# Optimization experiments

Measured on AMD Instinct MI355X. Metric: run time of the kernel, lower is better.

## Reference

```python
import jax, jax.numpy as jnp
import numpy as np

D = 1024
K_LOW1 = D // 4  # first low-precision segment of the contraction dim
K_LOW2 = D // 4  # last low-precision segment


def mix_precision_matmul(x, w):
    """x: [B,N,d], w: [d,3d]. Contraction dim d is split into
    low1 | high | low2 column bands; low bands run in fp16, high in fp32.
    Partial products are summed to give the full matmul result."""
    d = x.shape[-1]
    w1 = w[:K_LOW1]
    wh = w[K_LOW1:d - K_LOW2]
    w2 = w[d - K_LOW2:]
    y1 = jnp.matmul(x[..., :K_LOW1].astype(jnp.float16), w1.astype(jnp.float16)).astype(jnp.float32)
    yh = jnp.matmul(x[..., K_LOW1:d - K_LOW2], wh)
    y2 = jnp.matmul(x[..., d - K_LOW2:].astype(jnp.float16), w2.astype(jnp.float16)).astype(jnp.float32)
    return y1 + yh + y2


def setup_inputs() -> dict:
    key = jax.random.key(0)
    k1, k2, k3, k4 = jax.random.split(key, 4)
    B, N, d = 8, 2048, D
    x = jax.random.normal(k1, (B, N, d), dtype=jnp.float32)
    weight_qkv = jax.random.normal(k2, (d, 3 * d), dtype=jnp.float32) * (d ** -0.5)
    out_w = jax.random.normal(k3, (d, d), dtype=jnp.float32) * (d ** -0.5)
    out_b = jax.random.normal(k4, (d,), dtype=jnp.float32) * 0.01
    return {"x": x, "weight_qkv": weight_qkv, "out_w": out_w, "out_b": out_b}


def reference(x, weight_qkv, out_w, out_b):
    d = x.shape[-1]
    qkv = mix_precision_matmul(x, weight_qkv)  # [B, N, 3d]
    q, k, v = jnp.split(qkv, 3, axis=-1)
    q = q / jnp.sqrt(jnp.asarray(d, dtype=q.dtype))
    qk = jnp.einsum('bqd,bkd->bqk', q, k)      # [B, N, N]
    s = jax.nn.softmax(qk, axis=-1)
    y = jnp.einsum('bqk,bkd->bqd', s, v)       # [B, N, d]
    return jnp.matmul(y, out_w.T) + out_b
```

## Files before the change

kernel.cpp:

```cpp
#include <hip/hip_runtime.h>

typedef unsigned int u32;
typedef __attribute__((ext_vector_type(8))) _Float16 half8;
typedef __attribute__((ext_vector_type(4))) _Float16 half4;
typedef __attribute__((ext_vector_type(4))) float floatx4;

#define DEVI __device__ __forceinline__

DEVI void gload_lds16(const _Float16* g, _Float16* l) {
    __builtin_amdgcn_global_load_lds(
        (const __attribute__((address_space(1))) void*)g,
        (__attribute__((address_space(3))) void*)l, 16, 0, 0);
}

DEVI void stage128(const _Float16* __restrict__ g, int ldg, _Float16* lds, int tid) {
#pragma unroll
    for (int it = 0; it < 4; ++it) {
        int s = it * 256 + tid;
        int r = s >> 3, p = s & 7;
        int c = p ^ (r & 7);
        gload_lds16(g + (size_t)r * ldg + c * 8, lds + (size_t)s * 8);
    }
}

DEVI half8 frag(const _Float16* lds, int r, int ko) {
    return *(const half8*)&lds[r * 64 + (((ko >> 3) ^ (r & 7)) << 3)];
}

DEVI void mfma1_128(const _Float16* LA, const _Float16* LB,
                    floatx4 acc[4][4], int wm, int wn, int lane) {
    const int lr = lane & 15, quad = lane >> 4;
#pragma unroll
    for (int kk = 0; kk < 64; kk += 32) {
        const int ko = kk + quad * 8;
        half8 a[4], b[4];
#pragma unroll
        for (int i = 0; i < 4; ++i) {
            a[i] = frag(LA, wm * 64 + i * 16 + lr, ko);
            b[i] = frag(LB, wn * 64 + i * 16 + lr, ko);
        }
#pragma unroll
        for (int mi = 0; mi < 4; ++mi)
#pragma unroll
            for (int ni = 0; ni < 4; ++ni)
                acc[mi][ni] = __builtin_amdgcn_mfma_f32_16x16x32_f16(a[mi], b[ni], acc[mi][ni], 0, 0, 0);
    }
}

__global__ __launch_bounds__(256) void k_cast_x(const float* __restrict__ x, _Float16* __restrict__ xh) {
    size_t i = ((size_t)blockIdx.x * 256 + threadIdx.x) * 8;
    float4 v0 = *(const float4*)(x + i);
    float4 v1 = *(const float4*)(x + i + 4);
    float vv[8] = {v0.x, v0.y, v0.z, v0.w, v1.x, v1.y, v1.z, v1.w};
    half8 h;
#pragma unroll
    for (int j = 0; j < 8; ++j) h[j] = (_Float16)vv[j];
    *(half8*)(xh + i) = h;
}

__global__ __launch_bounds__(256) void k_prep_w(const float* __restrict__ w, _Float16* __restrict__ wh) {
    __shared__ float tile[32][33];
    const int n0 = blockIdx.x * 32, k0 = blockIdx.y * 32;
    const int t = threadIdx.x;
#pragma unroll
    for (int it = 0; it < 4; ++it) {
        int idx = it * 256 + t;
        int kk = idx >> 5, nn = idx & 31;
        tile[kk][nn] = w[(size_t)(k0 + kk) * 3072 + n0 + nn];
    }
    __syncthreads();
#pragma unroll
    for (int it = 0; it < 4; ++it) {
        int idx = it * 256 + t;
        int nn = idx >> 5, kk = idx & 31;
        wh[(size_t)(n0 + nn) * 1024 + k0 + kk] = (_Float16)tile[kk][nn];
    }
}

__global__ __launch_bounds__(256) void k_prep_ow(const float* __restrict__ ow, _Float16* __restrict__ owh) {
    size_t i = ((size_t)blockIdx.x * 256 + threadIdx.x) * 8;
    float4 v0 = *(const float4*)(ow + i);
    float4 v1 = *(const float4*)(ow + i + 4);
    float vv[8] = {v0.x, v0.y, v0.z, v0.w, v1.x, v1.y, v1.z, v1.w};
    half8 h;
#pragma unroll
    for (int j = 0; j < 8; ++j) h[j] = (_Float16)vv[j];
    *(half8*)(owh + i) = h;
}

__global__ __launch_bounds__(256, 3) void k_qkv(
    const _Float16* __restrict__ xh, const _Float16* __restrict__ wh,
    _Float16* __restrict__ qh, _Float16* __restrict__ kh, _Float16* __restrict__ vT)
{
    __shared__ __align__(16) _Float16 LA[128 * 64], LB[128 * 64];
    const int m0 = blockIdx.x * 128, n0 = blockIdx.y * 128;
    const int tid = threadIdx.x, lane = tid & 63, w = tid >> 6, wm = w >> 1, wn = w & 1;
    floatx4 acc[4][4];
    const floatx4 zf = {0.f, 0.f, 0.f, 0.f};
#pragma unroll
    for (int mi = 0; mi < 4; ++mi)
        for (int ni = 0; ni < 4; ++ni) acc[mi][ni] = zf;

    const _Float16* A = xh + (size_t)m0 * 1024;
    const _Float16* B = wh + (size_t)n0 * 1024;
    for (int kt = 0; kt < 16; ++kt) {
        stage128(A + kt * 64, 1024, LA, tid);
        stage128(B + kt * 64, 1024, LB, tid);
        __syncthreads();
        mfma1_128(LA, LB, acc, wm, wn, lane);
        __syncthreads();
    }

    const int lr = lane & 15, quad = lane >> 4;
    if (n0 < 1024) {
#pragma unroll
        for (int mi = 0; mi < 4; ++mi)
            for (int ni = 0; ni < 4; ++ni)
                for (int r = 0; r < 4; ++r) {
                    int m = m0 + wm * 64 + mi * 16 + quad * 4 + r;
                    int n = n0 + wn * 64 + ni * 16 + lr;
                    qh[(size_t)m * 1024 + n] = (_Float16)(acc[mi][ni][r] * 0.03125f);
                }
    } else if (n0 < 2048) {
#pragma unroll
        for (int mi = 0; mi < 4; ++mi)
            for (int ni = 0; ni < 4; ++ni)
                for (int r = 0; r < 4; ++r) {
                    int m = m0 + wm * 64 + mi * 16 + quad * 4 + r;
                    int n = n0 - 1024 + wn * 64 + ni * 16 + lr;
                    kh[(size_t)m * 1024 + n] = (_Float16)acc[mi][ni][r];
                }
    } else {
#pragma unroll
        for (int mi = 0; mi < 4; ++mi)
            for (int ni = 0; ni < 4; ++ni) {
                int mb = m0 + wm * 64 + mi * 16 + quad * 4;
                int b = mb >> 11, ml = mb & 2047;
                int e = n0 - 2048 + wn * 64 + ni * 16 + lr;
                half4 pk;
#pragma unroll
                for (int r = 0; r < 4; ++r) pk[r] = (_Float16)acc[mi][ni][r];
                *(half4*)&vT[((size_t)b * 1024 + e) * 2048 + ml] = pk;
            }
    }
}

template <int EPI>
__global__ __launch_bounds__(256, 3) void k_gemm128(
    const _Float16* __restrict__ Ab, const _Float16* __restrict__ Bb,
    _Float16* __restrict__ C16, float* __restrict__ C32, const float* __restrict__ bias,
    int K, unsigned long long sAz, unsigned long long sBz, unsigned long long sCz, int ldc)
{
    __shared__ __align__(16) _Float16 LA[128 * 64], LB[128 * 64];
    const int z = blockIdx.z;
    const int m0 = blockIdx.x * 128, n0 = blockIdx.y * 128;
    const _Float16* A = Ab + (size_t)z * sAz + (size_t)m0 * K;
    const _Float16* B = Bb + (size_t)z * sBz + (size_t)n0 * K;
    const int tid = threadIdx.x, lane = tid & 63, w = tid >> 6, wm = w >> 1, wn = w & 1;
    floatx4 acc[4][4];
    const floatx4 zf = {0.f, 0.f, 0.f, 0.f};
#pragma unroll
    for (int mi = 0; mi < 4; ++mi)
        for (int ni = 0; ni < 4; ++ni) acc[mi][ni] = zf;
    const int nkt = K >> 6;
    for (int kt = 0; kt < nkt; ++kt) {
        stage128(A + kt * 64, K, LA, tid);
        stage128(B + kt * 64, K, LB, tid);
        __syncthreads();
        mfma1_128(LA, LB, acc, wm, wn, lane);
        __syncthreads();
    }
    const int lr = lane & 15, quad = lane >> 4;
#pragma unroll
    for (int mi = 0; mi < 4; ++mi)
#pragma unroll
        for (int ni = 0; ni < 4; ++ni)
#pragma unroll
            for (int r = 0; r < 4; ++r) {
                int m = m0 + wm * 64 + mi * 16 + quad * 4 + r;
                int n = n0 + wn * 64 + ni * 16 + lr;
                if (EPI == 0)
                    C16[(size_t)z * sCz + (size_t)m * ldc + n] = (_Float16)acc[mi][ni][r];
                else
                    C32[(size_t)m * ldc + n] = acc[mi][ni][r] + bias[n];
            }
}

DEVI float wred_max(float v) {
#pragma unroll
    for (int o = 32; o; o >>= 1) v = fmaxf(v, __shfl_xor(v, o, 64));
    return v;
}
DEVI float wred_sum(float v) {
#pragma unroll
    for (int o = 32; o; o >>= 1) v += __shfl_xor(v, o, 64);
    return v;
}

__global__ __launch_bounds__(256) void k_softmax(_Float16* __restrict__ S) {
    const size_t row = blockIdx.x;
    _Float16* p = S + row * 2048;
    const int t = threadIdx.x;
    __shared__ float redm[4], reds[4];
    float v[8];
    float mx = -3.4e38f;
#pragma unroll
    for (int i = 0; i < 8; ++i) { v[i] = (float)p[t + i * 256]; mx = fmaxf(mx, v[i]); }
    mx = wred_max(mx);
    if ((t & 63) == 0) redm[t >> 6] = mx;
    __syncthreads();
    mx = fmaxf(fmaxf(redm[0], redm[1]), fmaxf(redm[2], redm[3]));
    float s = 0.f;
#pragma unroll
    for (int i = 0; i < 8; ++i) { v[i] = __expf(v[i] - mx); s += v[i]; }
    s = wred_sum(s);
    if ((t & 63) == 0) reds[t >> 6] = s;
    __syncthreads();
    s = reds[0] + reds[1] + reds[2] + reds[3];
    float inv = 1.0f / s;
#pragma unroll
    for (int i = 0; i < 8; ++i) p[t + i * 256] = (_Float16)(v[i] * inv);
}

extern "C" void kernel_launch(void* const* d_in, const int* in_sizes, int n_in,
                              void* d_out, int out_size, void* d_ws, size_t ws_size,
                              hipStream_t stream) {
    const float* x  = (const float*)d_in[0];
    const float* wq = (const float*)d_in[1];
    const float* ow = (const float*)d_in[2];
    const float* ob = (const float*)d_in[3];
    float* out = (float*)d_out;

    char* ws = (char*)d_ws;
    _Float16* xh  = (_Float16*)(ws + 0);
    _Float16* wh  = (_Float16*)(ws + 33554432);
    _Float16* S   = (_Float16*)(ws + 0);
    _Float16* qh  = (_Float16*)(ws + 67108864);
    _Float16* kh  = (_Float16*)(ws + 100663296);
    _Float16* vT  = (_Float16*)(ws + 134217728);
    _Float16* owh = (_Float16*)(ws + 167772160);
    _Float16* y   = qh;

    if (ws_size < 180355072ull) return;

    hipLaunchKernelGGL(k_cast_x, dim3(8192), dim3(256), 0, stream, x, xh);
    hipLaunchKernelGGL(k_prep_w, dim3(96, 32), dim3(256), 0, stream, wq, wh);
    hipLaunchKernelGGL(k_qkv, dim3(128, 24), dim3(256), 0, stream, xh, wh, qh, kh, vT);
    hipLaunchKernelGGL((k_gemm128<0>), dim3(16, 16, 8), dim3(256), 0, stream,
                       qh, kh, S, (float*)nullptr, (const float*)nullptr,
                       1024, 2048ull * 1024, 2048ull * 1024, 2048ull * 2048, 2048);
    hipLaunchKernelGGL(k_prep_ow, dim3(512), dim3(256), 0, stream, ow, owh);
    hipLaunchKernelGGL(k_softmax, dim3(16384), dim3(256), 0, stream, S);
    hipLaunchKernelGGL((k_gemm128<0>), dim3(16, 8, 8), dim3(256), 0, stream,
                       S, vT, y, (float*)nullptr, (const float*)nullptr,
                       2048, 2048ull * 2048, 1024ull * 2048, 2048ull * 1024, 1024);
    hipLaunchKernelGGL((k_gemm128<1>), dim3(128, 8, 1), dim3(256), 0, stream,
                       y, owh, (_Float16*)nullptr, out, ob,
                       1024, 0ull, 0ull, 0ull, 1024);
}
```

Measured before the change: 433.1 us.

## Merge prep kernels, swizzle GEMM tile order, vectorize softmax row access

Folds the three fp32-to-fp16 cast and transpose kernels into one launch that dispatches on block index. Remaps GEMM block IDs so groups of 8 M-tiles sweep together along N, for better L2 reuse of operand tiles. Switches softmax to a single 16-byte half8 load and store per thread instead of strided scalar accesses. Each thread's 8 elements are now contiguous, which does not change the row-wise softmax result. The swizzle may cost some reuse on grids where it falls back to the plain order.

```diff
diff --git a/kernel.cpp b/kernel.cpp
--- a/kernel.cpp
+++ b/kernel.cpp
@@ -47,45 +47,61 @@
     }
 }
 
-__global__ __launch_bounds__(256) void k_cast_x(const float* __restrict__ x, _Float16* __restrict__ xh) {
-    size_t i = ((size_t)blockIdx.x * 256 + threadIdx.x) * 8;
-    float4 v0 = *(const float4*)(x + i);
-    float4 v1 = *(const float4*)(x + i + 4);
-    float vv[8] = {v0.x, v0.y, v0.z, v0.w, v1.x, v1.y, v1.z, v1.w};
-    half8 h;
-#pragma unroll
-    for (int j = 0; j < 8; ++j) h[j] = (_Float16)vv[j];
-    *(half8*)(xh + i) = h;
-}
-
-__global__ __launch_bounds__(256) void k_prep_w(const float* __restrict__ w, _Float16* __restrict__ wh) {
+DEVI void swizzle_mn(int gx, int gy, int& mt, int& nt) {
+    int id = blockIdx.x + blockIdx.y * gx;
+    if ((gx & 7) == 0) {
+        int per = 8 * gy;
+        int chunk = id / per, rem = id % per;
+        mt = chunk * 8 + (rem & 7);
+        nt = rem >> 3;
+    } else {
+        mt = blockIdx.x; nt = blockIdx.y;
+    }
+}
+
+__global__ __launch_bounds__(256) void k_prep(
+    const float* __restrict__ x, _Float16* __restrict__ xh,
+    const float* __restrict__ wq, _Float16* __restrict__ wh,
+    const float* __restrict__ ow, _Float16* __restrict__ owh)
+{
     __shared__ float tile[32][33];
-    const int n0 = blockIdx.x * 32, k0 = blockIdx.y * 32;
-    const int t = threadIdx.x;
-#pragma unroll
-    for (int it = 0; it < 4; ++it) {
-        int idx = it * 256 + t;
-        int kk = idx >> 5, nn = idx & 31;
-        tile[kk][nn] = w[(size_t)(k0 + kk) * 3072 + n0 + nn];
-    }
-    __syncthreads();
-#pragma unroll
-    for (int it = 0; it < 4; ++it) {
-        int idx = it * 256 + t;
-        int nn = idx >> 5, kk = idx & 31;
-        wh[(size_t)(n0 + nn) * 1024 + k0 + kk] = (_Float16)tile[kk][nn];
-    }
-}
-
-__global__ __launch_bounds__(256) void k_prep_ow(const float* __restrict__ ow, _Float16* __restrict__ owh) {
-    size_t i = ((size_t)blockIdx.x * 256 + threadIdx.x) * 8;
-    float4 v0 = *(const float4*)(ow + i);
-    float4 v1 = *(const float4*)(ow + i + 4);
-    float vv[8] = {v0.x, v0.y, v0.z, v0.w, v1.x, v1.y, v1.z, v1.w};
-    half8 h;
-#pragma unroll
-    for (int j = 0; j < 8; ++j) h[j] = (_Float16)vv[j];
-    *(half8*)(owh + i) = h;
+    const int bid = blockIdx.x, t = threadIdx.x;
+    if (bid < 8192) {
+        size_t i = ((size_t)bid * 256 + t) * 8;
+        float4 v0 = *(const float4*)(x + i);
+        float4 v1 = *(const float4*)(x + i + 4);
+        float vv[8] = {v0.x, v0.y, v0.z, v0.w, v1.x, v1.y, v1.z, v1.w};
+        half8 h;
+#pragma unroll
+        for (int j = 0; j < 8; ++j) h[j] = (_Float16)vv[j];
+        *(half8*)(xh + i) = h;
+    } else if (bid < 11264) {
+        int id = bid - 8192;
+        const int n0 = (id % 96) * 32, k0 = (id / 96) * 32;
+#pragma unroll
+        for (int it = 0; it < 4; ++it) {
+            int idx = it * 256 + t;
+            int kk = idx >> 5, nn = idx & 31;
+            tile[kk][nn] = wq[(size_t)(k0 + kk) * 3072 + n0 + nn];
+        }
+        __syncthreads();
+#pragma unroll
+        for (int it = 0; it < 4; ++it) {
+            int idx = it * 256 + t;
+            int nn = idx >> 5, kk = idx & 31;
+            wh[(size_t)(n0 + nn) * 1024 + k0 + kk] = (_Float16)tile[kk][nn];
+        }
+    } else {
+        int id = bid - 11264;
+        size_t i = ((size_t)id * 256 + t) * 8;
+        float4 v0 = *(const float4*)(ow + i);
+        float4 v1 = *(const float4*)(ow + i + 4);
+        float vv[8] = {v0.x, v0.y, v0.z, v0.w, v1.x, v1.y, v1.z, v1.w};
+        half8 h;
+#pragma unroll
+        for (int j = 0; j < 8; ++j) h[j] = (_Float16)vv[j];
+        *(half8*)(owh + i) = h;
+    }
 }
 
 __global__ __launch_bounds__(256, 3) void k_qkv(
@@ -93,7 +109,9 @@
     _Float16* __restrict__ qh, _Float16* __restrict__ kh, _Float16* __restrict__ vT)
 {
     __shared__ __align__(16) _Float16 LA[128 * 64], LB[128 * 64];
-    const int m0 = blockIdx.x * 128, n0 = blockIdx.y * 128;
+    int mt, nt;
+    swizzle_mn(gridDim.x, gridDim.y, mt, nt);
+    const int m0 = mt * 128, n0 = nt * 128;
     const int tid = threadIdx.x, lane = tid & 63, w = tid >> 6, wm = w >> 1, wn = w & 1;
     floatx4 acc[4][4];
     const floatx4 zf = {0.f, 0.f, 0.f, 0.f};
@@ -153,7 +171,9 @@
 {
     __shared__ __align__(16) _Float16 LA[128 * 64], LB[128 * 64];
     const int z = blockIdx.z;
-    const int m0 = blockIdx.x * 128, n0 = blockIdx.y * 128;
+    int mt, nt;
+    swizzle_mn(gridDim.x, gridDim.y, mt, nt);
+    const int m0 = mt * 128, n0 = nt * 128;
     const _Float16* A = Ab + (size_t)z * sAz + (size_t)m0 * K;
     const _Float16* B = Bb + (size_t)z * sBz + (size_t)n0 * K;
     const int tid = threadIdx.x, lane = tid & 63, w = tid >> 6, wm = w >> 1, wn = w & 1;
@@ -202,10 +222,11 @@
     _Float16* p = S + row * 2048;
     const int t = threadIdx.x;
     __shared__ float redm[4], reds[4];
+    half8 hv = *(const half8*)(p + t * 8);
     float v[8];
     float mx = -3.4e38f;
 #pragma unroll
-    for (int i = 0; i < 8; ++i) { v[i] = (float)p[t + i * 256]; mx = fmaxf(mx, v[i]); }
+    for (int i = 0; i < 8; ++i) { v[i] = (float)hv[i]; mx = fmaxf(mx, v[i]); }
     mx = wred_max(mx);
     if ((t & 63) == 0) redm[t >> 6] = mx;
     __syncthreads();
@@ -219,7 +240,8 @@
     s = reds[0] + reds[1] + reds[2] + reds[3];
     float inv = 1.0f / s;
 #pragma unroll
-    for (int i = 0; i < 8; ++i) p[t + i * 256] = (_Float16)(v[i] * inv);
+    for (int i = 0; i < 8; ++i) hv[i] = (_Float16)(v[i] * inv);
+    *(half8*)(p + t * 8) = hv;
 }
 
 extern "C" void kernel_launch(void* const* d_in, const int* in_sizes, int n_in,
@@ -243,13 +265,11 @@
 
     if (ws_size < 180355072ull) return;
 
-    hipLaunchKernelGGL(k_cast_x, dim3(8192), dim3(256), 0, stream, x, xh);
-    hipLaunchKernelGGL(k_prep_w, dim3(96, 32), dim3(256), 0, stream, wq, wh);
+    hipLaunchKernelGGL(k_prep, dim3(11776), dim3(256), 0, stream, x, xh, wq, wh, ow, owh);
     hipLaunchKernelGGL(k_qkv, dim3(128, 24), dim3(256), 0, stream, xh, wh, qh, kh, vT);
     hipLaunchKernelGGL((k_gemm128<0>), dim3(16, 16, 8), dim3(256), 0, stream,
                        qh, kh, S, (float*)nullptr, (const float*)nullptr,
                        1024, 2048ull * 1024, 2048ull * 1024, 2048ull * 2048, 2048);
-    hipLaunchKernelGGL(k_prep_ow, dim3(512), dim3(256), 0, stream, ow, owh);
     hipLaunchKernelGGL(k_softmax, dim3(16384), dim3(256), 0, stream, S);
     hipLaunchKernelGGL((k_gemm128<0>), dim3(16, 8, 8), dim3(256), 0, stream,
                        S, vT, y, (float*)nullptr, (const float*)nullptr,
```

Result: slower. 452.6 us (+4.5%).
